# Kernel optimization log

Hardware: AMD Instinct MI355X
Metric: run time of the kernel (lower is better)

## Reference

```python
import jax, jax.numpy as jnp
import numpy as np

NF = 128   # n_feature
NA = 200000  # n_atoms
B = 256    # n_molecules (batch_mask rows)


def setup_inputs() -> dict:
    key = jax.random.key(0)
    ks = jax.random.split(key, 20)
    p = lambda k, shape: jax.random.normal(k, shape, jnp.float32) * 0.05
    s = jax.random.normal(ks[0], (1, NA, NF), jnp.float32)
    v = jax.random.normal(ks[1], (1, NA, 3, NF), jnp.float32)
    pos = jax.random.normal(ks[2], (1, NA, 3), jnp.float32)
    # one-hot batch mask: each atom assigned to one of B molecules
    idx = jax.random.randint(ks[3], (NA,), 0, B)
    batch = (idx[None, :] == jnp.arange(B)[:, None]).astype(jnp.float32)[..., None]  # (B, NA, 1)
    inp = dict(s=s, v=v, pos=pos, batch=batch)
    i = 4
    for l in range(2):  # n_output = 2 GatedEquivariant blocks
        inp[f"u{l}_w"] = p(ks[i], (NF, NF)); i += 1
        inp[f"v{l}_w"] = p(ks[i], (NF, NF)); i += 1
        inp[f"a{l}_w1"] = p(ks[i], (NF, 2 * NF)); i += 1
        inp[f"a{l}_b1"] = p(ks[i], (NF,)); i += 1
        inp[f"a{l}_w2"] = p(ks[i], (2 * NF, NF)); i += 1
        inp[f"a{l}_b2"] = p(ks[i], (2 * NF,)); i += 1
    inp["out_w"] = p(ks[i], (1, NF)); i += 1
    inp["out_b"] = p(ks[i], (1,))
    return inp


def _gated(s, v, uw, vw, aw1, ab1, aw2, ab2):
    # v: (1, na, 3, f); nn.Linear acts on last dim with weight (out, in)
    v1 = jnp.einsum('banf,gf->bang', v, uw)
    v2 = jnp.einsum('banf,gf->bang', v, vw)
    norm = jnp.linalg.norm(v2 + 1e-8, ord=2, axis=-2)  # (1, na, f)
    h = jnp.concatenate([s, norm], axis=-1)            # (1, na, 2f)
    h = jax.nn.silu(h @ aw1.T + ab1) @ aw2.T + ab2     # (1, na, 2f)
    sg, ss = jnp.split(h, 2, axis=-1)
    return sg, v1 * ss[:, :, None, :]


def reference(s, v, pos, batch,
              u0_w, v0_w, a0_w1, a0_b1, a0_w2, a0_b2,
              u1_w, v1_w, a1_w1, a1_b1, a1_w2, a1_b2,
              out_w, out_b):
    s, v = _gated(s, v, u0_w, v0_w, a0_w1, a0_b1, a0_w2, a0_b2)
    s, v = _gated(s, v, u1_w, v1_w, a1_w1, a1_b1, a1_w2, a1_b2)
    s = s @ out_w.T + out_b  # (1, na, 1)
    # faithful dense broadcast-mask pooling: (B, na, 1) * (B, na, 1) summed over atoms
    y = (jnp.broadcast_to(s, (batch.shape[0],) + s.shape[1:]) * batch).sum(axis=-2)
    return y  # (B, 1)
```

## Files before the change

kernel.cpp:

```cpp
#include <hip/hip_runtime.h>
#include <hip/hip_bf16.h>
#include <math.h>

typedef __attribute__((ext_vector_type(4))) float  f32x4;
typedef __attribute__((ext_vector_type(8))) __bf16 bf16x8;
typedef __attribute__((ext_vector_type(4))) unsigned int u32x4;

__device__ __forceinline__ unsigned short f2bu(float x) {
    __bf16 h = (__bf16)x;
    return __builtin_bit_cast(unsigned short, h);
}

__device__ __forceinline__ f32x4 MF(bf16x8 a, bf16x8 b, f32x4 c) {
    return __builtin_amdgcn_mfma_f32_16x16x32_bf16(a, b, c, 0, 0, 0);
}

__device__ __forceinline__ f32x4 zero4() { f32x4 z = {0.f, 0.f, 0.f, 0.f}; return z; }

__device__ __forceinline__ bf16x8 bfrag_g(const float* W, int ldk, int row, int k0) {
    const float* p = W + (size_t)row * ldk + k0;
    bf16x8 r;
#pragma unroll
    for (int e = 0; e < 8; ++e) r[e] = (__bf16)p[e];
    return r;
}

#define SET_SZ   20480
#define VIN_OFF  0
#define H_OFF    12288
#define S1_OFF   40960
#define RED_OFF  45056
#define LDS_BYTES 45568

__device__ __forceinline__ bf16x8 afrag(const unsigned char* base, int rb, int row, int kb) {
    u32x4 q = *(const u32x4*)(base + row * rb + (kb ^ ((row & 7) << 4)));
    return __builtin_bit_cast(bf16x8, q);
}

__device__ __forceinline__ unsigned long long pack4bf(f32x4 x) {
    return (unsigned long long)f2bu(x[0])
         | ((unsigned long long)f2bu(x[1]) << 16)
         | ((unsigned long long)f2bu(x[2]) << 32)
         | ((unsigned long long)f2bu(x[3]) << 48);
}

__global__ __launch_bounds__(512, 2) void eqsc_main(
    const float* __restrict__ S, const float* __restrict__ V,
    const float* __restrict__ u0w, const float* __restrict__ v0w,
    const float* __restrict__ a0w1, const float* __restrict__ a0b1,
    const float* __restrict__ a0w2, const float* __restrict__ a0b2,
    const float* __restrict__ u1w, const float* __restrict__ v1w,
    const float* __restrict__ a1w1, const float* __restrict__ a1b1,
    const float* __restrict__ a1w2, const float* __restrict__ a1b2,
    const float* __restrict__ outw, const float* __restrict__ outbp,
    float* __restrict__ sOut, int NT)
{
    __shared__ __align__(16) unsigned char lds[LDS_BYTES];
    const int tid  = threadIdx.x;
    const int lane = tid & 63;
    const int wv   = tid >> 6;
    const int l15  = lane & 15;
    const int lg   = lane >> 4;
    const int grow = wv * 16 + l15;
    const int kbb  = lg << 4;

    float wf = 0.f, cf = 0.f;
    for (int g = 0; g < 128; ++g) {
        float og = outw[g];
        wf += a1w2[g * 128 + grow] * og;
        cf += a1b2[g] * og;
    }
    cf += outbp[0];

    bf16x8 uw0f[4], vw0f[4], w2g0[4], w2s0[4], vw1f[4];
    bf16x8 w1f0[8], w1f1[8];
#pragma unroll
    for (int kt = 0; kt < 4; ++kt) {
        int k0 = kt * 32 + lg * 8;
        uw0f[kt] = bfrag_g(u0w, 128, grow, k0);
        vw0f[kt] = bfrag_g(v0w, 128, grow, k0);
        w2g0[kt] = bfrag_g(a0w2, 128, grow, k0);
        w2s0[kt] = bfrag_g(a0w2, 128, 128 + grow, k0);
        vw1f[kt] = bfrag_g(v1w, 128, grow, k0);
    }
#pragma unroll
    for (int kt = 0; kt < 8; ++kt) {
        int k0 = kt * 32 + lg * 8;
        w1f0[kt] = bfrag_g(a0w1, 256, grow, k0);
        w1f1[kt] = bfrag_g(a1w1, 256, grow, k0);
    }
    const float b1_0 = a0b1[grow];
    const float b2g0 = a0b2[grow];
    const float b2s0 = a0b2[128 + grow];
    const float b1_1 = a1b1[grow];

    const int stride = gridDim.x;
    const int t0 = blockIdx.x;

    {
        f32x4 vld[3], sld;
#pragma unroll
        for (int j = 0; j < 3; ++j) {
            int c = tid + (j << 9);
            int d = c >> 9, rem = c & 511;
            int row = rem >> 5, c4 = rem & 31;
            vld[j] = *(const f32x4*)(V + (((size_t)((t0 << 4) + row) * 3 + d) << 7) + (c4 << 2));
        }
        { int row = tid >> 5, c4 = tid & 31;
          sld = *(const f32x4*)(S + (((size_t)((t0 << 4) + row)) << 7) + (c4 << 2)); }
#pragma unroll
        for (int j = 0; j < 3; ++j) {
            int c = tid + (j << 9);
            int d = c >> 9, rem = c & 511;
            int row = rem >> 5, c4 = rem & 31;
            *(unsigned long long*)(lds + VIN_OFF + (d << 12) + row * 256 +
                                   ((c4 << 3) ^ ((row & 7) << 4))) = pack4bf(vld[j]);
        }
        { int row = tid >> 5, c4 = tid & 31;
          *(unsigned long long*)(lds + H_OFF + row * 512 +
                                 ((c4 << 3) ^ ((row & 7) << 4))) = pack4bf(sld); }
    }
    __syncthreads();

    int i = 0;
    for (int ty = t0; ty < NT + stride; ty += stride, ++i) {
        const bool yv = (ty < NT);
        const bool xv = (i > 0);
        const int  tz = ty + stride;
        const bool zv = (tz < NT);
        unsigned char* Lsy = lds + (i & 1) * SET_SZ;
        unsigned char* Lsx = lds + ((i & 1) ^ 1) * SET_SZ;

        f32x4 vld[3], sld;
        if (zv) {
#pragma unroll
            for (int j = 0; j < 3; ++j) {
                int c = tid + (j << 9);
                int d = c >> 9, rem = c & 511;
                int row = rem >> 5, c4 = rem & 31;
                vld[j] = *(const f32x4*)(V + (((size_t)((tz << 4) + row) * 3 + d) << 7) + (c4 << 2));
            }
            { int row = tid >> 5, c4 = tid & 31;
              sld = *(const f32x4*)(S + (((size_t)((tz << 4) + row)) << 7) + (c4 << 2)); }
        }

        f32x4 v1a[3];
        if (yv) {
            f32x4 n2 = zero4();
#pragma unroll
            for (int d = 0; d < 3; ++d) {
                f32x4 a1 = zero4(), a2 = zero4();
#pragma unroll
                for (int kt = 0; kt < 4; ++kt) {
                    bf16x8 a = afrag(Lsy + VIN_OFF + (d << 12), 256, l15, (kt << 6) + kbb);
                    a1 = MF(a, uw0f[kt], a1);
                    a2 = MF(a, vw0f[kt], a2);
                }
                v1a[d] = a1;
#pragma unroll
                for (int e = 0; e < 4; ++e) { float x = a2[e] + 1e-8f; n2[e] += x * x; }
            }
#pragma unroll
            for (int e = 0; e < 4; ++e) {
                int row = (lg << 2) + e;
                *(unsigned short*)(Lsy + H_OFF + row * 512 +
                    ((256 + (grow << 1)) ^ ((row & 7) << 4))) = f2bu(sqrtf(n2[e]));
            }
        }
        if (xv) {
            f32x4 n2 = zero4();
#pragma unroll
            for (int d = 0; d < 3; ++d) {
                f32x4 acc = zero4();
#pragma unroll
                for (int kt = 0; kt < 4; ++kt)
                    acc = MF(afrag(Lsx + VIN_OFF + (d << 12), 256, l15, (kt << 6) + kbb),
                             vw1f[kt], acc);
#pragma unroll
                for (int e = 0; e < 4; ++e) { float x = acc[e] + 1e-8f; n2[e] += x * x; }
            }
#pragma unroll
            for (int e = 0; e < 4; ++e) {
                int row = (lg << 2) + e;
                *(unsigned short*)(Lsx + H_OFF + row * 512 +
                    ((256 + (grow << 1)) ^ ((row & 7) << 4))) = f2bu(sqrtf(n2[e]));
            }
        }
        __syncthreads();

        if (yv) {
            f32x4 m = zero4();
#pragma unroll
            for (int kt = 0; kt < 8; ++kt)
                m = MF(afrag(Lsy + H_OFF, 512, l15, (kt << 6) + kbb), w1f0[kt], m);
#pragma unroll
            for (int e = 0; e < 4; ++e) {
                float x = m[e] + b1_0;
                float y = x / (1.f + __expf(-x));
                int row = (lg << 2) + e;
                *(unsigned short*)(lds + S1_OFF + row * 256 +
                    ((grow << 1) ^ ((row & 7) << 4))) = f2bu(y);
            }
        }
        if (xv) {
            f32x4 m = zero4();
#pragma unroll
            for (int kt = 0; kt < 8; ++kt)
                m = MF(afrag(Lsx + H_OFF, 512, l15, (kt << 6) + kbb), w1f1[kt], m);
            float p[4];
#pragma unroll
            for (int e = 0; e < 4; ++e) {
                float x = m[e] + b1_1;
                float y = x / (1.f + __expf(-x));
                p[e] = y * wf;
            }
#pragma unroll
            for (int off = 1; off < 16; off <<= 1) {
#pragma unroll
                for (int e = 0; e < 4; ++e) p[e] += __shfl_xor(p[e], off);
            }
            if (l15 == 0) {
#pragma unroll
                for (int e = 0; e < 4; ++e)
                    *((float*)(lds + RED_OFF) + (wv << 4) + (lg << 2) + e) = p[e];
            }
        }
        if (zv) {
#pragma unroll
            for (int j = 0; j < 3; ++j) {
                int c = tid + (j << 9);
                int d = c >> 9, rem = c & 511;
                int row = rem >> 5, c4 = rem & 31;
                *(unsigned long long*)(Lsx + VIN_OFF + (d << 12) + row * 256 +
                                       ((c4 << 3) ^ ((row & 7) << 4))) = pack4bf(vld[j]);
            }
        }
        __syncthreads();

        if (yv) {
            f32x4 sg = zero4(), ssa = zero4();
#pragma unroll
            for (int kt = 0; kt < 4; ++kt) {
                bf16x8 a = afrag(lds + S1_OFF, 256, l15, (kt << 6) + kbb);
                sg  = MF(a, w2g0[kt], sg);
                ssa = MF(a, w2s0[kt], ssa);
            }
#pragma unroll
            for (int e = 0; e < 4; ++e) {
                int row = (lg << 2) + e;
                int swz = (row & 7) << 4;
                *(unsigned short*)(Lsy + H_OFF + row * 512 + ((grow << 1) ^ swz)) = f2bu(sg[e] + b2g0);
                float ssv = ssa[e] + b2s0;
#pragma unroll
                for (int d = 0; d < 3; ++d)
                    *(unsigned short*)(Lsy + VIN_OFF + (d << 12) + row * 256 +
                        ((grow << 1) ^ swz)) = f2bu(v1a[d][e] * ssv);
            }
        }
        if (zv) {
            int row = tid >> 5, c4 = tid & 31;
            *(unsigned long long*)(Lsx + H_OFF + row * 512 +
                                   ((c4 << 3) ^ ((row & 7) << 4))) = pack4bf(sld);
        }
        if (xv && tid < 16) {
            float s = 0.f;
#pragma unroll
            for (int w = 0; w < 8; ++w) s += *((float*)(lds + RED_OFF) + (w << 4) + tid);
            sOut[((ty - stride) << 4) + tid] = s + cf;
        }
        __syncthreads();
    }
}

__global__ __launch_bounds__(256) void eqsc_pool(const float* __restrict__ batch,
                                                 const float* __restrict__ s,
                                                 float* __restrict__ out,
                                                 int NA, int B, int CH)
{
    int b  = blockIdx.x % B;
    int ch = blockIdx.x / B;
    int a0 = ch * CH;
    int a1 = min(a0 + CH, NA);
    const float* br = batch + (size_t)b * NA;
    float acc = 0.f;
    for (int a = a0 + (threadIdx.x << 2); a < a1; a += 256 * 4) {
        f32x4 bb = *(const f32x4*)(br + a);
        f32x4 sv = *(const f32x4*)(s + a);
        acc += bb[0] * sv[0] + bb[1] * sv[1] + bb[2] * sv[2] + bb[3] * sv[3];
    }
#pragma unroll
    for (int off = 32; off > 0; off >>= 1) acc += __shfl_down(acc, off);
    __shared__ float wsum[4];
    if ((threadIdx.x & 63) == 0) wsum[threadIdx.x >> 6] = acc;
    __syncthreads();
    if (threadIdx.x == 0) atomicAdd(&out[b], wsum[0] + wsum[1] + wsum[2] + wsum[3]);
}

extern "C" void kernel_launch(void* const* d_in, const int* in_sizes, int n_in,
                              void* d_out, int out_size, void* d_ws, size_t ws_size,
                              hipStream_t stream)
{
    const float* S     = (const float*)d_in[0];
    const float* V     = (const float*)d_in[1];
    const float* batch = (const float*)d_in[3];
    const float* u0w   = (const float*)d_in[4];
    const float* v0w   = (const float*)d_in[5];
    const float* a0w1  = (const float*)d_in[6];
    const float* a0b1  = (const float*)d_in[7];
    const float* a0w2  = (const float*)d_in[8];
    const float* a0b2  = (const float*)d_in[9];
    const float* u1w   = (const float*)d_in[10];
    const float* v1w   = (const float*)d_in[11];
    const float* a1w1  = (const float*)d_in[12];
    const float* a1b1  = (const float*)d_in[13];
    const float* a1w2  = (const float*)d_in[14];
    const float* a1b2  = (const float*)d_in[15];
    const float* outw  = (const float*)d_in[16];
    const float* outb  = (const float*)d_in[17];

    const int NA = in_sizes[0] / 128;
    const int NT = NA / 16;
    const int B  = in_sizes[3] / NA;
    float* sAtom = (float*)d_ws;

    hipMemsetAsync(d_out, 0, (size_t)out_size * sizeof(float), stream);

    eqsc_main<<<256, 512, 0, stream>>>(S, V, u0w, v0w, a0w1, a0b1, a0w2, a0b2,
                                       u1w, v1w, a1w1, a1b1, a1w2, a1b2,
                                       outw, outb, sAtom, NT);

    const int CH  = 16384;
    const int NCH = (NA + CH - 1) / CH;
    eqsc_pool<<<B * NCH, 256, 0, stream>>>(batch, sAtom, (float*)d_out, NA, B, CH);
}
```

Before: 276.7 us.

## Double atom tile to 32 rows and stage inputs via global_load_lds DMA

Each iteration now handles 32 atoms instead of 16, running two MFMA row blocks per stage, which halves the number of loop iterations and barriers. Input V/S tiles are copied straight into LDS staging buffers with global_load_lds and converted to swizzled bf16 in a later phase, instead of being held in registers across the compute stages. LDS use per block grows to about 153 KB, which likely prevents two blocks per CU despite the launch bounds, and register pressure from holding v1a for two row blocks also rises.

```diff
diff --git a/kernel.cpp b/kernel.cpp
--- a/kernel.cpp
+++ b/kernel.cpp
@@ -25,12 +25,14 @@
     return r;
 }
 
-#define SET_SZ   20480
+#define SET_SZ   40960
 #define VIN_OFF  0
-#define H_OFF    12288
-#define S1_OFF   40960
-#define RED_OFF  45056
-#define LDS_BYTES 45568
+#define H_OFF    24576
+#define S1_OFF   81920
+#define RED_OFF  90112
+#define VSTG     91136
+#define SSTG     140288
+#define LDS_BYTES 156672
 
 __device__ __forceinline__ bf16x8 afrag(const unsigned char* base, int rb, int row, int kb) {
     u32x4 q = *(const u32x4*)(base + row * rb + (kb ^ ((row & 7) << 4)));
@@ -42,6 +44,44 @@
          | ((unsigned long long)f2bu(x[1]) << 16)
          | ((unsigned long long)f2bu(x[2]) << 32)
          | ((unsigned long long)f2bu(x[3]) << 48);
+}
+
+__device__ __forceinline__ void issue_dma(const float* __restrict__ S,
+                                          const float* __restrict__ V,
+                                          int t, int tid, int wv,
+                                          unsigned char* lds) {
+    const float* vsrc = V + (size_t)t * (32 * 384);
+    const float* ssrc = S + (size_t)t * (32 * 128);
+#pragma unroll
+    for (int j = 0; j < 6; ++j)
+        __builtin_amdgcn_global_load_lds((const void*)(vsrc + ((tid + (j << 9)) << 2)),
+                                         (void*)(lds + VSTG + (j << 13) + (wv << 10)),
+                                         16, 0, 0);
+#pragma unroll
+    for (int j = 0; j < 2; ++j)
+        __builtin_amdgcn_global_load_lds((const void*)(ssrc + ((tid + (j << 9)) << 2)),
+                                         (void*)(lds + SSTG + (j << 13) + (wv << 10)),
+                                         16, 0, 0);
+}
+
+__device__ __forceinline__ void cvt_tile(unsigned char* lds, unsigned char* dstSet, int tid) {
+#pragma unroll
+    for (int j = 0; j < 6; ++j) {
+        int c = tid + (j << 9);
+        f32x4 x = *(const f32x4*)(lds + VSTG + (c << 4));
+        int row = c / 96, rem = c - row * 96;
+        int d = rem >> 5, c4 = rem & 31;
+        *(unsigned long long*)(dstSet + VIN_OFF + (d << 13) + row * 256 +
+                               ((c4 << 3) ^ ((row & 7) << 4))) = pack4bf(x);
+    }
+#pragma unroll
+    for (int j = 0; j < 2; ++j) {
+        int c = tid + (j << 9);
+        f32x4 x = *(const f32x4*)(lds + SSTG + (c << 4));
+        int row = c >> 5, c4 = c & 31;
+        *(unsigned long long*)(dstSet + H_OFF + row * 512 +
+                               ((c4 << 3) ^ ((row & 7) << 4))) = pack4bf(x);
+    }
 }
 
 __global__ __launch_bounds__(512, 2) void eqsc_main(
@@ -97,29 +137,9 @@
     const int stride = gridDim.x;
     const int t0 = blockIdx.x;
 
-    {
-        f32x4 vld[3], sld;
-#pragma unroll
-        for (int j = 0; j < 3; ++j) {
-            int c = tid + (j << 9);
-            int d = c >> 9, rem = c & 511;
-            int row = rem >> 5, c4 = rem & 31;
-            vld[j] = *(const f32x4*)(V + (((size_t)((t0 << 4) + row) * 3 + d) << 7) + (c4 << 2));
-        }
-        { int row = tid >> 5, c4 = tid & 31;
-          sld = *(const f32x4*)(S + (((size_t)((t0 << 4) + row)) << 7) + (c4 << 2)); }
-#pragma unroll
-        for (int j = 0; j < 3; ++j) {
-            int c = tid + (j << 9);
-            int d = c >> 9, rem = c & 511;
-            int row = rem >> 5, c4 = rem & 31;
-            *(unsigned long long*)(lds + VIN_OFF + (d << 12) + row * 256 +
-                                   ((c4 << 3) ^ ((row & 7) << 4))) = pack4bf(vld[j]);
-        }
-        { int row = tid >> 5, c4 = tid & 31;
-          *(unsigned long long*)(lds + H_OFF + row * 512 +
-                                 ((c4 << 3) ^ ((row & 7) << 4))) = pack4bf(sld); }
-    }
+    if (t0 < NT) issue_dma(S, V, t0, tid, wv, lds);
+    __syncthreads();
+    if (t0 < NT) cvt_tile(lds, lds, tid);
     __syncthreads();
 
     int i = 0;
@@ -131,142 +151,137 @@
         unsigned char* Lsy = lds + (i & 1) * SET_SZ;
         unsigned char* Lsx = lds + ((i & 1) ^ 1) * SET_SZ;
 
-        f32x4 vld[3], sld;
-        if (zv) {
-#pragma unroll
-            for (int j = 0; j < 3; ++j) {
-                int c = tid + (j << 9);
-                int d = c >> 9, rem = c & 511;
-                int row = rem >> 5, c4 = rem & 31;
-                vld[j] = *(const f32x4*)(V + (((size_t)((tz << 4) + row) * 3 + d) << 7) + (c4 << 2));
-            }
-            { int row = tid >> 5, c4 = tid & 31;
-              sld = *(const f32x4*)(S + (((size_t)((tz << 4) + row)) << 7) + (c4 << 2)); }
-        }
-
-        f32x4 v1a[3];
+        if (zv) issue_dma(S, V, tz, tid, wv, lds);
+
+        f32x4 v1a[2][3];
         if (yv) {
-            f32x4 n2 = zero4();
-#pragma unroll
-            for (int d = 0; d < 3; ++d) {
-                f32x4 a1 = zero4(), a2 = zero4();
+#pragma unroll
+            for (int m = 0; m < 2; ++m) {
+                const int mr = m << 4;
+                f32x4 n2 = zero4();
+#pragma unroll
+                for (int d = 0; d < 3; ++d) {
+                    f32x4 a1 = zero4(), a2 = zero4();
+#pragma unroll
+                    for (int kt = 0; kt < 4; ++kt) {
+                        bf16x8 a = afrag(Lsy + VIN_OFF + (d << 13), 256, mr + l15, (kt << 6) + kbb);
+                        a1 = MF(a, uw0f[kt], a1);
+                        a2 = MF(a, vw0f[kt], a2);
+                    }
+                    v1a[m][d] = a1;
+#pragma unroll
+                    for (int e = 0; e < 4; ++e) { float x = a2[e] + 1e-8f; n2[e] += x * x; }
+                }
+#pragma unroll
+                for (int e = 0; e < 4; ++e) {
+                    int row = mr + (lg << 2) + e;
+                    *(unsigned short*)(Lsy + H_OFF + row * 512 +
+                        ((256 + (grow << 1)) ^ ((row & 7) << 4))) = f2bu(sqrtf(n2[e]));
+                }
+            }
+        }
+        if (xv) {
+#pragma unroll
+            for (int m = 0; m < 2; ++m) {
+                const int mr = m << 4;
+                f32x4 n2 = zero4();
+#pragma unroll
+                for (int d = 0; d < 3; ++d) {
+                    f32x4 acc = zero4();
+#pragma unroll
+                    for (int kt = 0; kt < 4; ++kt)
+                        acc = MF(afrag(Lsx + VIN_OFF + (d << 13), 256, mr + l15, (kt << 6) + kbb),
+                                 vw1f[kt], acc);
+#pragma unroll
+                    for (int e = 0; e < 4; ++e) { float x = acc[e] + 1e-8f; n2[e] += x * x; }
+                }
+#pragma unroll
+                for (int e = 0; e < 4; ++e) {
+                    int row = mr + (lg << 2) + e;
+                    *(unsigned short*)(Lsx + H_OFF + row * 512 +
+                        ((256 + (grow << 1)) ^ ((row & 7) << 4))) = f2bu(sqrtf(n2[e]));
+                }
+            }
+        }
+        __syncthreads();
+
+        if (yv) {
+#pragma unroll
+            for (int m = 0; m < 2; ++m) {
+                const int mr = m << 4;
+                f32x4 acc = zero4();
+#pragma unroll
+                for (int kt = 0; kt < 8; ++kt)
+                    acc = MF(afrag(Lsy + H_OFF, 512, mr + l15, (kt << 6) + kbb), w1f0[kt], acc);
+#pragma unroll
+                for (int e = 0; e < 4; ++e) {
+                    float x = acc[e] + b1_0;
+                    float y = x / (1.f + __expf(-x));
+                    int row = mr + (lg << 2) + e;
+                    *(unsigned short*)(lds + S1_OFF + row * 256 +
+                        ((grow << 1) ^ ((row & 7) << 4))) = f2bu(y);
+                }
+            }
+        }
+        if (xv) {
+#pragma unroll
+            for (int m = 0; m < 2; ++m) {
+                const int mr = m << 4;
+                f32x4 acc = zero4();
+#pragma unroll
+                for (int kt = 0; kt < 8; ++kt)
+                    acc = MF(afrag(Lsx + H_OFF, 512, mr + l15, (kt << 6) + kbb), w1f1[kt], acc);
+                float p[4];
+#pragma unroll
+                for (int e = 0; e < 4; ++e) {
+                    float x = acc[e] + b1_1;
+                    float y = x / (1.f + __expf(-x));
+                    p[e] = y * wf;
+                }
+#pragma unroll
+                for (int off = 1; off < 16; off <<= 1) {
+#pragma unroll
+                    for (int e = 0; e < 4; ++e) p[e] += __shfl_xor(p[e], off);
+                }
+                if (l15 == 0) {
+#pragma unroll
+                    for (int e = 0; e < 4; ++e)
+                        *((float*)(lds + RED_OFF) + (wv << 5) + mr + (lg << 2) + e) = p[e];
+                }
+            }
+        }
+        __syncthreads();
+
+        if (yv) {
+#pragma unroll
+            for (int m = 0; m < 2; ++m) {
+                const int mr = m << 4;
+                f32x4 sg = zero4(), ssa = zero4();
 #pragma unroll
                 for (int kt = 0; kt < 4; ++kt) {
-                    bf16x8 a = afrag(Lsy + VIN_OFF + (d << 12), 256, l15, (kt << 6) + kbb);
-                    a1 = MF(a, uw0f[kt], a1);
-                    a2 = MF(a, vw0f[kt], a2);
-                }
-                v1a[d] = a1;
-#pragma unroll
-                for (int e = 0; e < 4; ++e) { float x = a2[e] + 1e-8f; n2[e] += x * x; }
-            }
-#pragma unroll
-            for (int e = 0; e < 4; ++e) {
-                int row = (lg << 2) + e;
-                *(unsigned short*)(Lsy + H_OFF + row * 512 +
-                    ((256 + (grow << 1)) ^ ((row & 7) << 4))) = f2bu(sqrtf(n2[e]));
-            }
-        }
-        if (xv) {
-            f32x4 n2 = zero4();
-#pragma unroll
-            for (int d = 0; d < 3; ++d) {
-                f32x4 acc = zero4();
-#pragma unroll
-                for (int kt = 0; kt < 4; ++kt)
-                    acc = MF(afrag(Lsx + VIN_OFF + (d << 12), 256, l15, (kt << 6) + kbb),
-                             vw1f[kt], acc);
-#pragma unroll
-                for (int e = 0; e < 4; ++e) { float x = acc[e] + 1e-8f; n2[e] += x * x; }
-            }
-#pragma unroll
-            for (int e = 0; e < 4; ++e) {
-                int row = (lg << 2) + e;
-                *(unsigned short*)(Lsx + H_OFF + row * 512 +
-                    ((256 + (grow << 1)) ^ ((row & 7) << 4))) = f2bu(sqrtf(n2[e]));
-            }
-        }
-        __syncthreads();
-
-        if (yv) {
-            f32x4 m = zero4();
-#pragma unroll
-            for (int kt = 0; kt < 8; ++kt)
-                m = MF(afrag(Lsy + H_OFF, 512, l15, (kt << 6) + kbb), w1f0[kt], m);
-#pragma unroll
-            for (int e = 0; e < 4; ++e) {
-                float x = m[e] + b1_0;
-                float y = x / (1.f + __expf(-x));
-                int row = (lg << 2) + e;
-                *(unsigned short*)(lds + S1_OFF + row * 256 +
-                    ((grow << 1) ^ ((row & 7) << 4))) = f2bu(y);
-            }
-        }
-        if (xv) {
-            f32x4 m = zero4();
-#pragma unroll
-            for (int kt = 0; kt < 8; ++kt)
-                m = MF(afrag(Lsx + H_OFF, 512, l15, (kt << 6) + kbb), w1f1[kt], m);
-            float p[4];
-#pragma unroll
-            for (int e = 0; e < 4; ++e) {
-                float x = m[e] + b1_1;
-                float y = x / (1.f + __expf(-x));
-                p[e] = y * wf;
-            }
-#pragma unroll
-            for (int off = 1; off < 16; off <<= 1) {
-#pragma unroll
-                for (int e = 0; e < 4; ++e) p[e] += __shfl_xor(p[e], off);
-            }
-            if (l15 == 0) {
-#pragma unroll
-                for (int e = 0; e < 4; ++e)
-                    *((float*)(lds + RED_OFF) + (wv << 4) + (lg << 2) + e) = p[e];
-            }
-        }
-        if (zv) {
-#pragma unroll
-            for (int j = 0; j < 3; ++j) {
-                int c = tid + (j << 9);
-                int d = c >> 9, rem = c & 511;
-                int row = rem >> 5, c4 = rem & 31;
-                *(unsigned long long*)(Lsx + VIN_OFF + (d << 12) + row * 256 +
-                                       ((c4 << 3) ^ ((row & 7) << 4))) = pack4bf(vld[j]);
-            }
-        }
-        __syncthreads();
-
-        if (yv) {
-            f32x4 sg = zero4(), ssa = zero4();
-#pragma unroll
-            for (int kt = 0; kt < 4; ++kt) {
-                bf16x8 a = afrag(lds + S1_OFF, 256, l15, (kt << 6) + kbb);
-                sg  = MF(a, w2g0[kt], sg);
-                ssa = MF(a, w2s0[kt], ssa);
-            }
-#pragma unroll
-            for (int e = 0; e < 4; ++e) {
-                int row = (lg << 2) + e;
-                int swz = (row & 7) << 4;
-                *(unsigned short*)(Lsy + H_OFF + row * 512 + ((grow << 1) ^ swz)) = f2bu(sg[e] + b2g0);
-                float ssv = ssa[e] + b2s0;
-#pragma unroll
-                for (int d = 0; d < 3; ++d)
-                    *(unsigned short*)(Lsy + VIN_OFF + (d << 12) + row * 256 +
-                        ((grow << 1) ^ swz)) = f2bu(v1a[d][e] * ssv);
-            }
-        }
-        if (zv) {
-            int row = tid >> 5, c4 = tid & 31;
-            *(unsigned long long*)(Lsx + H_OFF + row * 512 +
-                                   ((c4 << 3) ^ ((row & 7) << 4))) = pack4bf(sld);
-        }
-        if (xv && tid < 16) {
+                    bf16x8 a = afrag(lds + S1_OFF, 256, mr + l15, (kt << 6) + kbb);
+                    sg  = MF(a, w2g0[kt], sg);
+                    ssa = MF(a, w2s0[kt], ssa);
+                }
+#pragma unroll
+                for (int e = 0; e < 4; ++e) {
+                    int row = mr + (lg << 2) + e;
+                    int swz = (row & 7) << 4;
+                    *(unsigned short*)(Lsy + H_OFF + row * 512 + ((grow << 1) ^ swz)) = f2bu(sg[e] + b2g0);
+                    float ssv = ssa[e] + b2s0;
+#pragma unroll
+                    for (int d = 0; d < 3; ++d)
+                        *(unsigned short*)(Lsy + VIN_OFF + (d << 13) + row * 256 +
+                            ((grow << 1) ^ swz)) = f2bu(v1a[m][d][e] * ssv);
+                }
+            }
+        }
+        if (zv) cvt_tile(lds, Lsx, tid);
+        if (xv && tid < 32) {
             float s = 0.f;
 #pragma unroll
-            for (int w = 0; w < 8; ++w) s += *((float*)(lds + RED_OFF) + (w << 4) + tid);
-            sOut[((ty - stride) << 4) + tid] = s + cf;
+            for (int w = 0; w < 8; ++w) s += *((float*)(lds + RED_OFF) + (w << 5) + tid);
+            sOut[((ty - stride) << 5) + tid] = s + cf;
         }
         __syncthreads();
     }
@@ -319,7 +334,7 @@
     const float* outb  = (const float*)d_in[17];
 
     const int NA = in_sizes[0] / 128;
-    const int NT = NA / 16;
+    const int NT = NA / 32;
     const int B  = in_sizes[3] / NA;
     float* sAtom = (float*)d_ws;
 
```

Measured after the change: 424.3 us. 1.53x slower.

## Deepen software pipeline to three LDS tile sets with two barriers per iteration

Applied to the files above, without the earlier changes.

Restructures the persistent main loop from a two-stage double-buffered pipeline with three barriers per iteration into a four-stage schedule over three rotating LDS tile sets, with two barriers per iteration. The v1 partial results are now stashed in LDS instead of being held in registers across stages. V loads for the next tile are issued after the first barrier, and the S load for the current tile moves into the same iteration. The goal is fewer barriers per tile and more independent MFMA work between syncs to hide global-load latency. In exchange, LDS use grows to about 115 KB, which with launch_bounds(512,2) may exceed the per-CU LDS budget and reduce occupancy to one block.

```diff
diff --git a/kernel.cpp b/kernel.cpp
--- a/kernel.cpp
+++ b/kernel.cpp
@@ -25,12 +25,14 @@
     return r;
 }
 
-#define SET_SZ   20480
-#define VIN_OFF  0
-#define H_OFF    12288
-#define S1_OFF   40960
-#define RED_OFF  45056
-#define LDS_BYTES 45568
+#define SET_SZ    20480
+#define VIN_OFF   0
+#define H_OFF     12288
+#define S1_OFF    61440
+#define RED_OFF   65536
+#define STASH_OFF 66048
+#define STASH_SZ  24576
+#define LDS_BYTES 115200
 
 __device__ __forceinline__ bf16x8 afrag(const unsigned char* base, int rb, int row, int kb) {
     u32x4 q = *(const u32x4*)(base + row * rb + (kb ^ ((row & 7) << 4)));
@@ -42,6 +44,22 @@
          | ((unsigned long long)f2bu(x[1]) << 16)
          | ((unsigned long long)f2bu(x[2]) << 32)
          | ((unsigned long long)f2bu(x[3]) << 48);
+}
+
+__device__ __forceinline__ void load_v(const float* __restrict__ V, int t, int tid, f32x4* vld) {
+    const float* vsrc = V + (size_t)t * (16 * 384);
+#pragma unroll
+    for (int j = 0; j < 3; ++j) vld[j] = *(const f32x4*)(vsrc + ((tid + (j << 9)) << 2));
+}
+__device__ __forceinline__ void write_v(unsigned char* dstSet, int tid, const f32x4* vld) {
+#pragma unroll
+    for (int j = 0; j < 3; ++j) {
+        int c = tid + (j << 9);
+        int row = c / 96, rem = c - row * 96;
+        int d = rem >> 5, c4 = rem & 31;
+        *(unsigned long long*)(dstSet + VIN_OFF + (d << 12) + row * 256 +
+                               ((c4 << 3) ^ ((row & 7) << 4))) = pack4bf(vld[j]);
+    }
 }
 
 __global__ __launch_bounds__(512, 2) void eqsc_main(
@@ -58,10 +76,10 @@
     __shared__ __align__(16) unsigned char lds[LDS_BYTES];
     const int tid  = threadIdx.x;
     const int lane = tid & 63;
-    const int wv   = tid >> 6;
+    const int wvv  = tid >> 6;
     const int l15  = lane & 15;
     const int lg   = lane >> 4;
-    const int grow = wv * 16 + l15;
+    const int grow = wvv * 16 + l15;
     const int kbb  = lg << 4;
 
     float wf = 0.f, cf = 0.f;
@@ -96,55 +114,37 @@
 
     const int stride = gridDim.x;
     const int t0 = blockIdx.x;
+    const int NI = (NT - t0 + stride - 1) / stride;
 
     {
-        f32x4 vld[3], sld;
-#pragma unroll
-        for (int j = 0; j < 3; ++j) {
-            int c = tid + (j << 9);
-            int d = c >> 9, rem = c & 511;
-            int row = rem >> 5, c4 = rem & 31;
-            vld[j] = *(const f32x4*)(V + (((size_t)((t0 << 4) + row) * 3 + d) << 7) + (c4 << 2));
-        }
-        { int row = tid >> 5, c4 = tid & 31;
-          sld = *(const f32x4*)(S + (((size_t)((t0 << 4) + row)) << 7) + (c4 << 2)); }
-#pragma unroll
-        for (int j = 0; j < 3; ++j) {
-            int c = tid + (j << 9);
-            int d = c >> 9, rem = c & 511;
-            int row = rem >> 5, c4 = rem & 31;
-            *(unsigned long long*)(lds + VIN_OFF + (d << 12) + row * 256 +
-                                   ((c4 << 3) ^ ((row & 7) << 4))) = pack4bf(vld[j]);
-        }
-        { int row = tid >> 5, c4 = tid & 31;
-          *(unsigned long long*)(lds + H_OFF + row * 512 +
-                                 ((c4 << 3) ^ ((row & 7) << 4))) = pack4bf(sld); }
+        f32x4 vld[3];
+        load_v(V, t0, tid, vld);
+        write_v(lds, tid, vld);
     }
     __syncthreads();
 
-    int i = 0;
-    for (int ty = t0; ty < NT + stride; ty += stride, ++i) {
-        const bool yv = (ty < NT);
-        const bool xv = (i > 0);
-        const int  tz = ty + stride;
-        const bool zv = (tz < NT);
-        unsigned char* Lsy = lds + (i & 1) * SET_SZ;
-        unsigned char* Lsx = lds + ((i & 1) ^ 1) * SET_SZ;
-
-        f32x4 vld[3], sld;
-        if (zv) {
-#pragma unroll
-            for (int j = 0; j < 3; ++j) {
-                int c = tid + (j << 9);
-                int d = c >> 9, rem = c & 511;
-                int row = rem >> 5, c4 = rem & 31;
-                vld[j] = *(const f32x4*)(V + (((size_t)((tz << 4) + row) * 3 + d) << 7) + (c4 << 2));
-            }
-            { int row = tid >> 5, c4 = tid & 31;
-              sld = *(const f32x4*)(S + (((size_t)((tz << 4) + row)) << 7) + (c4 << 2)); }
-        }
-
-        f32x4 v1a[3];
+    for (int i = 0; i < NI + 3; ++i) {
+        const int ty = t0 + i * stride;
+        const bool yv = (i < NI);
+        const bool xvd = (i >= 1) && (i - 1 < NI);
+        const bool wvd = (i >= 2) && (i - 2 < NI);
+        const bool fvd = (i >= 3) && (i - 3 < NI);
+        const bool zvd = (i + 1 < NI);
+        unsigned char* setY = lds + (i % 3) * SET_SZ;
+        unsigned char* setX = lds + ((i + 2) % 3) * SET_SZ;
+        unsigned char* setW = lds + ((i + 1) % 3) * SET_SZ;
+        unsigned char* stashY = lds + STASH_OFF + (i & 1) * STASH_SZ + wvv * 3072 + (lane << 4);
+        unsigned char* stashX = lds + STASH_OFF + ((i & 1) ^ 1) * STASH_SZ + wvv * 3072 + (lane << 4);
+
+        if (fvd && tid < 16) {
+            float s = 0.f;
+#pragma unroll
+            for (int w = 0; w < 8; ++w) s += *((float*)(lds + RED_OFF) + (w << 4) + tid);
+            sOut[((t0 + (i - 3) * stride) << 4) + tid] = s + cf;
+        }
+        f32x4 sldY;
+        if (yv) sldY = *(const f32x4*)(S + (size_t)ty * (16 * 128) + (tid << 2));
+
         if (yv) {
             f32x4 n2 = zero4();
 #pragma unroll
@@ -152,65 +152,98 @@
                 f32x4 a1 = zero4(), a2 = zero4();
 #pragma unroll
                 for (int kt = 0; kt < 4; ++kt) {
-                    bf16x8 a = afrag(Lsy + VIN_OFF + (d << 12), 256, l15, (kt << 6) + kbb);
+                    bf16x8 a = afrag(setY + VIN_OFF + (d << 12), 256, l15, (kt << 6) + kbb);
                     a1 = MF(a, uw0f[kt], a1);
                     a2 = MF(a, vw0f[kt], a2);
                 }
-                v1a[d] = a1;
+                *(f32x4*)(stashY + (d << 10)) = a1;
 #pragma unroll
                 for (int e = 0; e < 4; ++e) { float x = a2[e] + 1e-8f; n2[e] += x * x; }
             }
 #pragma unroll
             for (int e = 0; e < 4; ++e) {
                 int row = (lg << 2) + e;
-                *(unsigned short*)(Lsy + H_OFF + row * 512 +
+                *(unsigned short*)(setY + H_OFF + row * 512 +
                     ((256 + (grow << 1)) ^ ((row & 7) << 4))) = f2bu(sqrtf(n2[e]));
             }
         }
-        if (xv) {
-            f32x4 n2 = zero4();
+        if (xvd) {
+            f32x4 sg = zero4(), ssa = zero4();
+#pragma unroll
+            for (int kt = 0; kt < 4; ++kt) {
+                bf16x8 a = afrag(lds + S1_OFF, 256, l15, (kt << 6) + kbb);
+                sg  = MF(a, w2g0[kt], sg);
+                ssa = MF(a, w2s0[kt], ssa);
+            }
+#pragma unroll
+            for (int e = 0; e < 4; ++e) {
+                int row = (lg << 2) + e;
+                *(unsigned short*)(setX + H_OFF + row * 512 +
+                    ((grow << 1) ^ ((row & 7) << 4))) = f2bu(sg[e] + b2g0);
+            }
 #pragma unroll
             for (int d = 0; d < 3; ++d) {
-                f32x4 acc = zero4();
-#pragma unroll
-                for (int kt = 0; kt < 4; ++kt)
-                    acc = MF(afrag(Lsx + VIN_OFF + (d << 12), 256, l15, (kt << 6) + kbb),
-                             vw1f[kt], acc);
-#pragma unroll
-                for (int e = 0; e < 4; ++e) { float x = acc[e] + 1e-8f; n2[e] += x * x; }
-            }
-#pragma unroll
-            for (int e = 0; e < 4; ++e) {
-                int row = (lg << 2) + e;
-                *(unsigned short*)(Lsx + H_OFF + row * 512 +
-                    ((256 + (grow << 1)) ^ ((row & 7) << 4))) = f2bu(sqrtf(n2[e]));
-            }
+                f32x4 v1 = *(const f32x4*)(stashX + (d << 10));
+#pragma unroll
+                for (int e = 0; e < 4; ++e) {
+                    int row = (lg << 2) + e;
+                    *(unsigned short*)(setX + VIN_OFF + (d << 12) + row * 256 +
+                        ((grow << 1) ^ ((row & 7) << 4))) = f2bu(v1[e] * (ssa[e] + b2s0));
+                }
+            }
+        }
+        if (yv) {
+            int row = tid >> 5, c4 = tid & 31;
+            *(unsigned long long*)(setY + H_OFF + row * 512 +
+                                   ((c4 << 3) ^ ((row & 7) << 4))) = pack4bf(sldY);
         }
         __syncthreads();
 
+        f32x4 vldZ[3];
+        if (zvd) load_v(V, ty + stride, tid, vldZ);
+
         if (yv) {
-            f32x4 m = zero4();
+            f32x4 acc = zero4();
 #pragma unroll
             for (int kt = 0; kt < 8; ++kt)
-                m = MF(afrag(Lsy + H_OFF, 512, l15, (kt << 6) + kbb), w1f0[kt], m);
-#pragma unroll
-            for (int e = 0; e < 4; ++e) {
-                float x = m[e] + b1_0;
+                acc = MF(afrag(setY + H_OFF, 512, l15, (kt << 6) + kbb), w1f0[kt], acc);
+#pragma unroll
+            for (int e = 0; e < 4; ++e) {
+                float x = acc[e] + b1_0;
                 float y = x / (1.f + __expf(-x));
                 int row = (lg << 2) + e;
                 *(unsigned short*)(lds + S1_OFF + row * 256 +
                     ((grow << 1) ^ ((row & 7) << 4))) = f2bu(y);
             }
         }
-        if (xv) {
-            f32x4 m = zero4();
+        if (xvd) {
+            f32x4 n2 = zero4();
+#pragma unroll
+            for (int d = 0; d < 3; ++d) {
+                f32x4 acc = zero4();
+#pragma unroll
+                for (int kt = 0; kt < 4; ++kt)
+                    acc = MF(afrag(setX + VIN_OFF + (d << 12), 256, l15, (kt << 6) + kbb),
+                             vw1f[kt], acc);
+#pragma unroll
+                for (int e = 0; e < 4; ++e) { float x = acc[e] + 1e-8f; n2[e] += x * x; }
+            }
+#pragma unroll
+            for (int e = 0; e < 4; ++e) {
+                int row = (lg << 2) + e;
+                *(unsigned short*)(setX + H_OFF + row * 512 +
+                    ((256 + (grow << 1)) ^ ((row & 7) << 4))) = f2bu(sqrtf(n2[e]));
+            }
+        }
+        if (wvd) {
+            f32x4 acc = zero4();
 #pragma unroll
             for (int kt = 0; kt < 8; ++kt)
-                m = MF(afrag(Lsx + H_OFF, 512, l15, (kt << 6) + kbb), w1f1[kt], m);
+                acc = MF(afrag(setW + H_OFF, 512, l15, (kt << 6) + kbb), w1f1[kt], acc);
             float p[4];
 #pragma unroll
             for (int e = 0; e < 4; ++e) {
-                float x = m[e] + b1_1;
+                float x = acc[e] + b1_1;
                 float y = x / (1.f + __expf(-x));
                 p[e] = y * wf;
             }
@@ -222,52 +255,10 @@
             if (l15 == 0) {
 #pragma unroll
                 for (int e = 0; e < 4; ++e)
-                    *((float*)(lds + RED_OFF) + (wv << 4) + (lg << 2) + e) = p[e];
-            }
-        }
-        if (zv) {
-#pragma unroll
-            for (int j = 0; j < 3; ++j) {
-                int c = tid + (j << 9);
-                int d = c >> 9, rem = c & 511;
-                int row = rem >> 5, c4 = rem & 31;
-                *(unsigned long long*)(Lsx + VIN_OFF + (d << 12) + row * 256 +
-                                       ((c4 << 3) ^ ((row & 7) << 4))) = pack4bf(vld[j]);
-            }
-        }
-        __syncthreads();
-
-        if (yv) {
-            f32x4 sg = zero4(), ssa = zero4();
-#pragma unroll
-            for (int kt = 0; kt < 4; ++kt) {
-                bf16x8 a = afrag(lds + S1_OFF, 256, l15, (kt << 6) + kbb);
-                sg  = MF(a, w2g0[kt], sg);
-                ssa = MF(a, w2s0[kt], ssa);
-            }
-#pragma unroll
-            for (int e = 0; e < 4; ++e) {
-                int row = (lg << 2) + e;
-                int swz = (row & 7) << 4;
-                *(unsigned short*)(Lsy + H_OFF + row * 512 + ((grow << 1) ^ swz)) = f2bu(sg[e] + b2g0);
-                float ssv = ssa[e] + b2s0;
-#pragma unroll
-                for (int d = 0; d < 3; ++d)
-                    *(unsigned short*)(Lsy + VIN_OFF + (d << 12) + row * 256 +
-                        ((grow << 1) ^ swz)) = f2bu(v1a[d][e] * ssv);
-            }
-        }
-        if (zv) {
-            int row = tid >> 5, c4 = tid & 31;
-            *(unsigned long long*)(Lsx + H_OFF + row * 512 +
-                                   ((c4 << 3) ^ ((row & 7) << 4))) = pack4bf(sld);
-        }
-        if (xv && tid < 16) {
-            float s = 0.f;
-#pragma unroll
-            for (int w = 0; w < 8; ++w) s += *((float*)(lds + RED_OFF) + (w << 4) + tid);
-            sOut[((ty - stride) << 4) + tid] = s + cf;
-        }
+                    *((float*)(lds + RED_OFF) + (wvv << 4) + (lg << 2) + e) = p[e];
+            }
+        }
+        if (zvd) write_v(setW, tid, vldZ);
         __syncthreads();
     }
 }
```

After: 384.4 us. 38.9% more time.

## Pre-convert weights to bf16 in workspace, load B fragments from memory, use 4-wave blocks

Applied to the files above, without the earlier changes.

Adds a prep kernel that converts the weight matrices to bf16 once and precomputes the folded output weights and bias into workspace. The main kernel no longer keeps all weight fragments in registers and instead reads bf16 B fragments from global/L2 on every MFMA. Each wave now covers 32 output columns (two 16-col halves), and the launch becomes 768 blocks of 256 threads with an occupancy hint of 3. The goal is to free registers and raise occupancy, at the cost of repeated weight loads from cache in the inner loops and one extra kernel launch.

```diff
diff --git a/kernel.cpp b/kernel.cpp
--- a/kernel.cpp
+++ b/kernel.cpp
@@ -17,12 +17,9 @@
 
 __device__ __forceinline__ f32x4 zero4() { f32x4 z = {0.f, 0.f, 0.f, 0.f}; return z; }
 
-__device__ __forceinline__ bf16x8 bfrag_g(const float* W, int ldk, int row, int k0) {
-    const float* p = W + (size_t)row * ldk + k0;
-    bf16x8 r;
-#pragma unroll
-    for (int e = 0; e < 8; ++e) r[e] = (__bf16)p[e];
-    return r;
+__device__ __forceinline__ bf16x8 bfragb(const unsigned short* __restrict__ w,
+                                         int ldk, int row, int k0) {
+    return __builtin_bit_cast(bf16x8, *(const u32x4*)(w + row * ldk + k0));
 }
 
 #define SET_SZ   20480
@@ -32,6 +29,10 @@
 #define RED_OFF  45056
 #define LDS_BYTES 45568
 
+#define WFOLD_BYTE 294912
+#define CF_BYTE    295424
+#define SATOM_BYTE 295936
+
 __device__ __forceinline__ bf16x8 afrag(const unsigned char* base, int rb, int row, int kb) {
     u32x4 q = *(const u32x4*)(base + row * rb + (kb ^ ((row & 7) << 4)));
     return __builtin_bit_cast(bf16x8, q);
@@ -44,15 +45,71 @@
          | ((unsigned long long)f2bu(x[3]) << 48);
 }
 
-__global__ __launch_bounds__(512, 2) void eqsc_main(
+__device__ __forceinline__ void load_v6(const float* __restrict__ V, int t, int tid, f32x4* vld) {
+    const float* p = V + (size_t)t * 6144;
+#pragma unroll
+    for (int j = 0; j < 6; ++j) vld[j] = *(const f32x4*)(p + ((tid + (j << 8)) << 2));
+}
+__device__ __forceinline__ void write_v6(unsigned char* dst, int tid, const f32x4* vld) {
+#pragma unroll
+    for (int j = 0; j < 6; ++j) {
+        int c = tid + (j << 8);
+        int row = c / 96, rem = c - row * 96;
+        int d = rem >> 5, c4 = rem & 31;
+        *(unsigned long long*)(dst + VIN_OFF + (d << 12) + row * 256 +
+                               ((c4 << 3) ^ ((row & 7) << 4))) = pack4bf(vld[j]);
+    }
+}
+__device__ __forceinline__ void load_s2(const float* __restrict__ S, int t, int tid, f32x4* sld) {
+    const float* p = S + (size_t)t * 2048;
+#pragma unroll
+    for (int j = 0; j < 2; ++j) sld[j] = *(const f32x4*)(p + ((tid + (j << 8)) << 2));
+}
+__device__ __forceinline__ void write_s2(unsigned char* dst, int tid, const f32x4* sld) {
+#pragma unroll
+    for (int j = 0; j < 2; ++j) {
+        int c = tid + (j << 8);
+        int row = c >> 5, c4 = c & 31;
+        *(unsigned long long*)(dst + H_OFF + row * 512 +
+                               ((c4 << 3) ^ ((row & 7) << 4))) = pack4bf(sld[j]);
+    }
+}
+
+__global__ __launch_bounds__(256) void eqsc_prep(
+    const float* __restrict__ u0w, const float* __restrict__ v0w,
+    const float* __restrict__ a0w2, const float* __restrict__ v1w,
+    const float* __restrict__ a0w1, const float* __restrict__ a1w1,
+    const float* __restrict__ a1w2, const float* __restrict__ outw,
+    const float* __restrict__ a1b2, const float* __restrict__ outbp,
+    unsigned short* __restrict__ wb, float* __restrict__ wfold, float* __restrict__ cfp)
+{
+    int i = blockIdx.x * 256 + threadIdx.x;
+    float v;
+    if (i < 16384)       v = u0w[i];
+    else if (i < 32768)  v = v0w[i - 16384];
+    else if (i < 65536)  v = a0w2[i - 32768];
+    else if (i < 81920)  v = v1w[i - 65536];
+    else if (i < 114688) v = a0w1[i - 81920];
+    else                 v = a1w1[i - 114688];
+    wb[i] = f2bu(v);
+    if (blockIdx.x == 0 && threadIdx.x < 128) {
+        float wf = 0.f;
+        for (int g = 0; g < 128; ++g) wf += a1w2[g * 128 + threadIdx.x] * outw[g];
+        wfold[threadIdx.x] = wf;
+        if (threadIdx.x == 0) {
+            float c = 0.f;
+            for (int g = 0; g < 128; ++g) c += a1b2[g] * outw[g];
+            cfp[0] = c + outbp[0];
+        }
+    }
+}
+
+__global__ __launch_bounds__(256, 3) void eqsc_main(
     const float* __restrict__ S, const float* __restrict__ V,
-    const float* __restrict__ u0w, const float* __restrict__ v0w,
-    const float* __restrict__ a0w1, const float* __restrict__ a0b1,
-    const float* __restrict__ a0w2, const float* __restrict__ a0b2,
-    const float* __restrict__ u1w, const float* __restrict__ v1w,
-    const float* __restrict__ a1w1, const float* __restrict__ a1b1,
-    const float* __restrict__ a1w2, const float* __restrict__ a1b2,
-    const float* __restrict__ outw, const float* __restrict__ outbp,
+    const unsigned short* __restrict__ wb,
+    const float* __restrict__ wfold, const float* __restrict__ cfp,
+    const float* __restrict__ a0b1, const float* __restrict__ a0b2,
+    const float* __restrict__ a1b1,
     float* __restrict__ sOut, int NT)
 {
     __shared__ __align__(16) unsigned char lds[LDS_BYTES];
@@ -61,64 +118,34 @@
     const int wv   = tid >> 6;
     const int l15  = lane & 15;
     const int lg   = lane >> 4;
-    const int grow = wv * 16 + l15;
-    const int kbb  = lg << 4;
-
-    float wf = 0.f, cf = 0.f;
-    for (int g = 0; g < 128; ++g) {
-        float og = outw[g];
-        wf += a1w2[g * 128 + grow] * og;
-        cf += a1b2[g] * og;
-    }
-    cf += outbp[0];
-
-    bf16x8 uw0f[4], vw0f[4], w2g0[4], w2s0[4], vw1f[4];
-    bf16x8 w1f0[8], w1f1[8];
-#pragma unroll
-    for (int kt = 0; kt < 4; ++kt) {
-        int k0 = kt * 32 + lg * 8;
-        uw0f[kt] = bfrag_g(u0w, 128, grow, k0);
-        vw0f[kt] = bfrag_g(v0w, 128, grow, k0);
-        w2g0[kt] = bfrag_g(a0w2, 128, grow, k0);
-        w2s0[kt] = bfrag_g(a0w2, 128, 128 + grow, k0);
-        vw1f[kt] = bfrag_g(v1w, 128, grow, k0);
-    }
-#pragma unroll
-    for (int kt = 0; kt < 8; ++kt) {
-        int k0 = kt * 32 + lg * 8;
-        w1f0[kt] = bfrag_g(a0w1, 256, grow, k0);
-        w1f1[kt] = bfrag_g(a1w1, 256, grow, k0);
-    }
-    const float b1_0 = a0b1[grow];
-    const float b2g0 = a0b2[grow];
-    const float b2s0 = a0b2[128 + grow];
-    const float b1_1 = a1b1[grow];
+    const int gA   = wv * 32 + l15;
+    const int gB   = gA + 16;
+    float* red = (float*)(lds + RED_OFF);
+
+    const unsigned short* u0wB  = wb;
+    const unsigned short* v0wB  = wb + 16384;
+    const unsigned short* w2gB  = wb + 32768;
+    const unsigned short* w2sB  = wb + 49152;
+    const unsigned short* v1wB  = wb + 65536;
+    const unsigned short* w1f0B = wb + 81920;
+    const unsigned short* w1f1B = wb + 114688;
+
+    const float b1_0A = a0b1[gA],       b1_0B = a0b1[gB];
+    const float b2g0A = a0b2[gA],       b2g0B = a0b2[gB];
+    const float b2s0A = a0b2[128 + gA], b2s0B = a0b2[128 + gB];
+    const float b1_1A = a1b1[gA],       b1_1B = a1b1[gB];
+    const float wfA   = wfold[gA],      wfB   = wfold[gB];
+    const float cf    = cfp[0];
 
     const int stride = gridDim.x;
     const int t0 = blockIdx.x;
 
     {
-        f32x4 vld[3], sld;
-#pragma unroll
-        for (int j = 0; j < 3; ++j) {
-            int c = tid + (j << 9);
-            int d = c >> 9, rem = c & 511;
-            int row = rem >> 5, c4 = rem & 31;
-            vld[j] = *(const f32x4*)(V + (((size_t)((t0 << 4) + row) * 3 + d) << 7) + (c4 << 2));
-        }
-        { int row = tid >> 5, c4 = tid & 31;
-          sld = *(const f32x4*)(S + (((size_t)((t0 << 4) + row)) << 7) + (c4 << 2)); }
-#pragma unroll
-        for (int j = 0; j < 3; ++j) {
-            int c = tid + (j << 9);
-            int d = c >> 9, rem = c & 511;
-            int row = rem >> 5, c4 = rem & 31;
-            *(unsigned long long*)(lds + VIN_OFF + (d << 12) + row * 256 +
-                                   ((c4 << 3) ^ ((row & 7) << 4))) = pack4bf(vld[j]);
-        }
-        { int row = tid >> 5, c4 = tid & 31;
-          *(unsigned long long*)(lds + H_OFF + row * 512 +
-                                 ((c4 << 3) ^ ((row & 7) << 4))) = pack4bf(sld); }
+        f32x4 vld[6], sld[2];
+        load_v6(V, t0, tid, vld);
+        load_s2(S, t0, tid, sld);
+        write_v6(lds, tid, vld);
+        write_s2(lds, tid, sld);
     }
     __syncthreads();
 
@@ -131,141 +158,148 @@
         unsigned char* Lsy = lds + (i & 1) * SET_SZ;
         unsigned char* Lsx = lds + ((i & 1) ^ 1) * SET_SZ;
 
-        f32x4 vld[3], sld;
-        if (zv) {
-#pragma unroll
-            for (int j = 0; j < 3; ++j) {
-                int c = tid + (j << 9);
-                int d = c >> 9, rem = c & 511;
-                int row = rem >> 5, c4 = rem & 31;
-                vld[j] = *(const f32x4*)(V + (((size_t)((tz << 4) + row) * 3 + d) << 7) + (c4 << 2));
-            }
-            { int row = tid >> 5, c4 = tid & 31;
-              sld = *(const f32x4*)(S + (((size_t)((tz << 4) + row)) << 7) + (c4 << 2)); }
-        }
-
-        f32x4 v1a[3];
+        f32x4 vldZ[6], sldZ[2];
+        if (zv) { load_v6(V, tz, tid, vldZ); load_s2(S, tz, tid, sldZ); }
+
+        f32x4 v1aA[3], v1aB[3];
         if (yv) {
-            f32x4 n2 = zero4();
+            f32x4 n2A = zero4(), n2B = zero4();
 #pragma unroll
             for (int d = 0; d < 3; ++d) {
-                f32x4 a1 = zero4(), a2 = zero4();
+                f32x4 uA = zero4(), uB = zero4(), vA = zero4(), vB = zero4();
 #pragma unroll
                 for (int kt = 0; kt < 4; ++kt) {
-                    bf16x8 a = afrag(Lsy + VIN_OFF + (d << 12), 256, l15, (kt << 6) + kbb);
-                    a1 = MF(a, uw0f[kt], a1);
-                    a2 = MF(a, vw0f[kt], a2);
-                }
-                v1a[d] = a1;
-#pragma unroll
-                for (int e = 0; e < 4; ++e) { float x = a2[e] + 1e-8f; n2[e] += x * x; }
-            }
-#pragma unroll
-            for (int e = 0; e < 4; ++e) {
-                int row = (lg << 2) + e;
-                *(unsigned short*)(Lsy + H_OFF + row * 512 +
-                    ((256 + (grow << 1)) ^ ((row & 7) << 4))) = f2bu(sqrtf(n2[e]));
+                    const int k0 = kt * 32 + lg * 8;
+                    bf16x8 a = afrag(Lsy + VIN_OFF + (d << 12), 256, l15, (kt << 6) + (lg << 4));
+                    uA = MF(a, bfragb(u0wB, 128, gA, k0), uA);
+                    uB = MF(a, bfragb(u0wB, 128, gB, k0), uB);
+                    vA = MF(a, bfragb(v0wB, 128, gA, k0), vA);
+                    vB = MF(a, bfragb(v0wB, 128, gB, k0), vB);
+                }
+                v1aA[d] = uA; v1aB[d] = uB;
+#pragma unroll
+                for (int e = 0; e < 4; ++e) {
+                    float xA = vA[e] + 1e-8f; n2A[e] += xA * xA;
+                    float xB = vB[e] + 1e-8f; n2B[e] += xB * xB;
+                }
+            }
+#pragma unroll
+            for (int e = 0; e < 4; ++e) {
+                int row = (lg << 2) + e, swz = (row & 7) << 4;
+                *(unsigned short*)(Lsy + H_OFF + row * 512 + ((256 + (gA << 1)) ^ swz)) = f2bu(sqrtf(n2A[e]));
+                *(unsigned short*)(Lsy + H_OFF + row * 512 + ((256 + (gB << 1)) ^ swz)) = f2bu(sqrtf(n2B[e]));
             }
         }
         if (xv) {
-            f32x4 n2 = zero4();
+            f32x4 n2A = zero4(), n2B = zero4();
 #pragma unroll
             for (int d = 0; d < 3; ++d) {
-                f32x4 acc = zero4();
-#pragma unroll
-                for (int kt = 0; kt < 4; ++kt)
-                    acc = MF(afrag(Lsx + VIN_OFF + (d << 12), 256, l15, (kt << 6) + kbb),
-                             vw1f[kt], acc);
-#pragma unroll
-                for (int e = 0; e < 4; ++e) { float x = acc[e] + 1e-8f; n2[e] += x * x; }
-            }
-#pragma unroll
-            for (int e = 0; e < 4; ++e) {
-                int row = (lg << 2) + e;
-                *(unsigned short*)(Lsx + H_OFF + row * 512 +
-                    ((256 + (grow << 1)) ^ ((row & 7) << 4))) = f2bu(sqrtf(n2[e]));
+                f32x4 aA = zero4(), aB = zero4();
+#pragma unroll
+                for (int kt = 0; kt < 4; ++kt) {
+                    const int k0 = kt * 32 + lg * 8;
+                    bf16x8 a = afrag(Lsx + VIN_OFF + (d << 12), 256, l15, (kt << 6) + (lg << 4));
+                    aA = MF(a, bfragb(v1wB, 128, gA, k0), aA);
+                    aB = MF(a, bfragb(v1wB, 128, gB, k0), aB);
+                }
+#pragma unroll
+                for (int e = 0; e < 4; ++e) {
+                    float xA = aA[e] + 1e-8f; n2A[e] += xA * xA;
+                    float xB = aB[e] + 1e-8f; n2B[e] += xB * xB;
+                }
+            }
+#pragma unroll
+            for (int e = 0; e < 4; ++e) {
+                int row = (lg << 2) + e, swz = (row & 7) << 4;
+                *(unsigned short*)(Lsx + H_OFF + row * 512 + ((256 + (gA << 1)) ^ swz)) = f2bu(sqrtf(n2A[e]));
+                *(unsigned short*)(Lsx + H_OFF + row * 512 + ((256 + (gB << 1)) ^ swz)) = f2bu(sqrtf(n2B[e]));
             }
         }
         __syncthreads();
 
         if (yv) {
-            f32x4 m = zero4();
-#pragma unroll
-            for (int kt = 0; kt < 8; ++kt)
-                m = MF(afrag(Lsy + H_OFF, 512, l15, (kt << 6) + kbb), w1f0[kt], m);
-#pragma unroll
-            for (int e = 0; e < 4; ++e) {
-                float x = m[e] + b1_0;
-                float y = x / (1.f + __expf(-x));
-                int row = (lg << 2) + e;
-                *(unsigned short*)(lds + S1_OFF + row * 256 +
-                    ((grow << 1) ^ ((row & 7) << 4))) = f2bu(y);
+            f32x4 mA = zero4(), mB = zero4();
+#pragma unroll
+            for (int kt = 0; kt < 8; ++kt) {
+                const int k0 = kt * 32 + lg * 8;
+                bf16x8 a = afrag(Lsy + H_OFF, 512, l15, (kt << 6) + (lg << 4));
+                mA = MF(a, bfragb(w1f0B, 256, gA, k0), mA);
+                mB = MF(a, bfragb(w1f0B, 256, gB, k0), mB);
+            }
+#pragma unroll
+            for (int e = 0; e < 4; ++e) {
+                int row = (lg << 2) + e, swz = (row & 7) << 4;
+                float xA = mA[e] + b1_0A, xB = mB[e] + b1_0B;
+                *(unsigned short*)(lds + S1_OFF + row * 256 + ((gA << 1) ^ swz)) = f2bu(xA / (1.f + __expf(-xA)));
+                *(unsigned short*)(lds + S1_OFF + row * 256 + ((gB << 1) ^ swz)) = f2bu(xB / (1.f + __expf(-xB)));
             }
         }
         if (xv) {
-            f32x4 m = zero4();
-#pragma unroll
-            for (int kt = 0; kt < 8; ++kt)
-                m = MF(afrag(Lsx + H_OFF, 512, l15, (kt << 6) + kbb), w1f1[kt], m);
-            float p[4];
-#pragma unroll
-            for (int e = 0; e < 4; ++e) {
-                float x = m[e] + b1_1;
-                float y = x / (1.f + __expf(-x));
-                p[e] = y * wf;
+            f32x4 mA = zero4(), mB = zero4();
+#pragma unroll
+            for (int kt = 0; kt < 8; ++kt) {
+                const int k0 = kt * 32 + lg * 8;
+                bf16x8 a = afrag(Lsx + H_OFF, 512, l15, (kt << 6) + (lg << 4));
+                mA = MF(a, bfragb(w1f1B, 256, gA, k0), mA);
+                mB = MF(a, bfragb(w1f1B, 256, gB, k0), mB);
+            }
+            float pA[4], pB[4];
+#pragma unroll
+            for (int e = 0; e < 4; ++e) {
+                float xA = mA[e] + b1_1A, xB = mB[e] + b1_1B;
+                pA[e] = (xA / (1.f + __expf(-xA))) * wfA;
+                pB[e] = (xB / (1.f + __expf(-xB))) * wfB;
             }
 #pragma unroll
             for (int off = 1; off < 16; off <<= 1) {
 #pragma unroll
-                for (int e = 0; e < 4; ++e) p[e] += __shfl_xor(p[e], off);
+                for (int e = 0; e < 4; ++e) {
+                    pA[e] += __shfl_xor(pA[e], off);
+                    pB[e] += __shfl_xor(pB[e], off);
+                }
             }
             if (l15 == 0) {
 #pragma unroll
-                for (int e = 0; e < 4; ++e)
-                    *((float*)(lds + RED_OFF) + (wv << 4) + (lg << 2) + e) = p[e];
-            }
-        }
-        if (zv) {
-#pragma unroll
-            for (int j = 0; j < 3; ++j) {
-                int c = tid + (j << 9);
-                int d = c >> 9, rem = c & 511;
-                int row = rem >> 5, c4 = rem & 31;
-                *(unsigned long long*)(Lsx + VIN_OFF + (d << 12) + row * 256 +
-                                       ((c4 << 3) ^ ((row & 7) << 4))) = pack4bf(vld[j]);
-            }
-        }
+                for (int e = 0; e < 4; ++e) {
+                    red[((wv << 1) + 0) * 16 + (lg << 2) + e] = pA[e];
+                    red[((wv << 1) + 1) * 16 + (lg << 2) + e] = pB[e];
+                }
+            }
+        }
+        if (zv) write_v6(Lsx, tid, vldZ);
         __syncthreads();
 
         if (yv) {
-            f32x4 sg = zero4(), ssa = zero4();
+            f32x4 sgA = zero4(), sgB = zero4(), ssA = zero4(), ssB = zero4();
 #pragma unroll
             for (int kt = 0; kt < 4; ++kt) {
-                bf16x8 a = afrag(lds + S1_OFF, 256, l15, (kt << 6) + kbb);
-                sg  = MF(a, w2g0[kt], sg);
-                ssa = MF(a, w2s0[kt], ssa);
-            }
-#pragma unroll
-            for (int e = 0; e < 4; ++e) {
-                int row = (lg << 2) + e;
-                int swz = (row & 7) << 4;
-                *(unsigned short*)(Lsy + H_OFF + row * 512 + ((grow << 1) ^ swz)) = f2bu(sg[e] + b2g0);
-                float ssv = ssa[e] + b2s0;
-#pragma unroll
-                for (int d = 0; d < 3; ++d)
-                    *(unsigned short*)(Lsy + VIN_OFF + (d << 12) + row * 256 +
-                        ((grow << 1) ^ swz)) = f2bu(v1a[d][e] * ssv);
-            }
-        }
-        if (zv) {
-            int row = tid >> 5, c4 = tid & 31;
-            *(unsigned long long*)(Lsx + H_OFF + row * 512 +
-                                   ((c4 << 3) ^ ((row & 7) << 4))) = pack4bf(sld);
-        }
+                const int k0 = kt * 32 + lg * 8;
+                bf16x8 a = afrag(lds + S1_OFF, 256, l15, (kt << 6) + (lg << 4));
+                sgA = MF(a, bfragb(w2gB, 128, gA, k0), sgA);
+                sgB = MF(a, bfragb(w2gB, 128, gB, k0), sgB);
+                ssA = MF(a, bfragb(w2sB, 128, gA, k0), ssA);
+                ssB = MF(a, bfragb(w2sB, 128, gB, k0), ssB);
+            }
+#pragma unroll
+            for (int e = 0; e < 4; ++e) {
+                int row = (lg << 2) + e, swz = (row & 7) << 4;
+                *(unsigned short*)(Lsy + H_OFF + row * 512 + ((gA << 1) ^ swz)) = f2bu(sgA[e] + b2g0A);
+                *(unsigned short*)(Lsy + H_OFF + row * 512 + ((gB << 1) ^ swz)) = f2bu(sgB[e] + b2g0B);
+                float ssvA = ssA[e] + b2s0A, ssvB = ssB[e] + b2s0B;
+#pragma unroll
+                for (int d = 0; d < 3; ++d) {
+                    *(unsigned short*)(Lsy + VIN_OFF + (d << 12) + row * 256 + ((gA << 1) ^ swz)) =
+                        f2bu(v1aA[d][e] * ssvA);
+                    *(unsigned short*)(Lsy + VIN_OFF + (d << 12) + row * 256 + ((gB << 1) ^ swz)) =
+                        f2bu(v1aB[d][e] * ssvB);
+                }
+            }
+        }
+        if (zv) write_s2(Lsx, tid, sldZ);
         if (xv && tid < 16) {
             float s = 0.f;
 #pragma unroll
-            for (int w = 0; w < 8; ++w) s += *((float*)(lds + RED_OFF) + (w << 4) + tid);
+            for (int g = 0; g < 8; ++g) s += red[g * 16 + tid];
             sOut[((ty - stride) << 4) + tid] = s + cf;
         }
         __syncthreads();
@@ -317,17 +351,24 @@
     const float* a1b2  = (const float*)d_in[15];
     const float* outw  = (const float*)d_in[16];
     const float* outb  = (const float*)d_in[17];
+    (void)u1w;
 
     const int NA = in_sizes[0] / 128;
     const int NT = NA / 16;
     const int B  = in_sizes[3] / NA;
-    float* sAtom = (float*)d_ws;
+
+    unsigned short* wbuf = (unsigned short*)d_ws;
+    float* wfold = (float*)((char*)d_ws + WFOLD_BYTE);
+    float* cfp   = (float*)((char*)d_ws + CF_BYTE);
+    float* sAtom = (float*)((char*)d_ws + SATOM_BYTE);
 
     hipMemsetAsync(d_out, 0, (size_t)out_size * sizeof(float), stream);
 
-    eqsc_main<<<256, 512, 0, stream>>>(S, V, u0w, v0w, a0w1, a0b1, a0w2, a0b2,
-                                       u1w, v1w, a1w1, a1b1, a1w2, a1b2,
-                                       outw, outb, sAtom, NT);
+    eqsc_prep<<<576, 256, 0, stream>>>(u0w, v0w, a0w2, v1w, a0w1, a1w1,
+                                       a1w2, outw, a1b2, outb, wbuf, wfold, cfp);
+
+    eqsc_main<<<768, 256, 0, stream>>>(S, V, wbuf, wfold, cfp,
+                                       a0b1, a0b2, a1b1, sAtom, NT);
 
     const int CH  = 16384;
     const int NCH = (NA + CH - 1) / CH;
```

Measured after the change: 698.4 us. 2.52x slower.
